# Kernel optimization log

Measured on AMD Instinct MI355X. Metric: run time of the kernel, lower is better.

Reference implementation:

```python
import jax, jax.numpy as jnp
import numpy as np

D_MODEL = 1024


def setup_inputs() -> dict:
    key = jax.random.key(0)
    ks = jax.random.split(key, 7)
    B, S, D = 4, 2048, D_MODEL
    scale = 1.0 / np.sqrt(D)
    inp = {
        "query": jax.random.normal(ks[0], (B, S, D), dtype=jnp.float32),
        "key": jax.random.normal(ks[1], (B, S, D), dtype=jnp.float32),
        "value": jax.random.normal(ks[2], (B, S, D), dtype=jnp.float32),
        # NOTE: original torch code applies query_projection to q, k AND v,
        # so only one projection weight (Wq) participates, plus output proj.
        "Wq": (jax.random.normal(ks[3], (D, D), dtype=jnp.float32) * scale),
        "bq": jnp.zeros((D,), dtype=jnp.float32),
        "Wo": (jax.random.normal(ks[4], (D, D), dtype=jnp.float32) * scale),
        "bo": jnp.zeros((D,), dtype=jnp.float32),
    }
    return inp


def reference(query, key, value, Wq, bq, Wo, bo):
    # Faithful to source: same projection (Wq, bq) used for q, k, v.
    q = jnp.einsum("bsd,de->bse", query, Wq) + bq   # (B, S, D)
    k = jnp.einsum("btd,de->bte", key, Wq) + bq     # (B, T, D)
    v = jnp.einsum("btd,de->bte", value, Wq) + bq   # (B, T, D)
    # No 1/sqrt(d) scaling in the original.
    score = jnp.einsum("bse,bte->bst", q, k)        # (B, S, T)
    weights = jax.nn.softmax(score, axis=-1)
    # Dropout is identity in eval / for a deterministic reference.
    ctx = jnp.einsum("bst,bte->bse", weights, v)    # (B, S, D)
    out = jnp.einsum("bse,ef->bsf", ctx, Wo) + bo   # (B, S, D)
    return (out, weights)
```

## Files before the change

kernel.cpp:

```cpp
#include <hip/hip_runtime.h>

typedef unsigned short u16;
typedef unsigned int u32;
typedef signed char i8;
typedef __bf16 bf16x8 __attribute__((ext_vector_type(8)));
typedef float f32x4 __attribute__((ext_vector_type(4)));
typedef int i32x4 __attribute__((ext_vector_type(4)));
typedef i8 i8x4 __attribute__((ext_vector_type(4)));
typedef u16 u16x8 __attribute__((ext_vector_type(8)));

#define AS1(p) ((const __attribute__((address_space(1))) void*)(p))
#define AS3(p) ((__attribute__((address_space(3))) void*)(p))

__device__ __forceinline__ u16 f2bf(float x) {
  u32 u = __float_as_uint(x);
  u32 r = u + 0x7fffu + ((u >> 16) & 1u);
  return (u16)(r >> 16);
}
__device__ __forceinline__ float bf2f(u16 h) {
  return __uint_as_float(((u32)h) << 16);
}

#define S_IN (8.0f / 127.0f)
#define S_W (0.25f / 127.0f)
#define S_QK (8.0f / 127.0f)
#define INV_S_IN (127.0f / 8.0f)
#define INV_S_W (508.0f)
#define INV_S_QK (127.0f / 8.0f)

__device__ __forceinline__ int2 q8i(float x, float inv_s) {
  float t = fminf(fmaxf(x * inv_s, -126.99f), 126.99f);
  float hf = rintf(t);
  float lf = fminf(fmaxf(rintf((t - hf) * 256.0f), -127.0f), 127.0f);
  return make_int2((int)hf, (int)lf);
}

__global__ __launch_bounds__(256) void prep_all(
    const float* __restrict__ q, const float* __restrict__ k,
    const float* __restrict__ value, const float* __restrict__ Wq,
    const float* __restrict__ Wo, i8* __restrict__ qh, i8* __restrict__ ql,
    i8* __restrict__ kh, i8* __restrict__ kl, u16* __restrict__ valT,
    i8* __restrict__ wqt_h, i8* __restrict__ wqt_l, u16* __restrict__ wot,
    u16* __restrict__ wq_b) {
  __shared__ float tileA[32][33];
  __shared__ float tileB[32][33];
  const int bid = blockIdx.x;
  const int tid = threadIdx.x;
  const int D = 1024;

  if (bid < 8192) {
    const int bx = bid & 31;
    const int by = (bid >> 5) & 63;
    const int bz = bid >> 11;
    const int tx = tid & 31, ty = tid >> 5;
    const int c0 = bx * 32, r0 = by * 32;
    const size_t zi = (size_t)bz * 2048 * 1024;
#pragma unroll
    for (int i = ty; i < 32; i += 8)
      tileA[i][tx] = value[zi + (size_t)(r0 + i) * D + (c0 + tx)];
    __syncthreads();
#pragma unroll
    for (int i = ty; i < 32; i += 8)
      valT[zi + (size_t)(c0 + i) * 2048 + (r0 + tx)] = f2bf(tileA[tx][i]);
  } else if (bid < 10240) {
    const int b2 = bid - 8192;
    const int n4 = 2097152;
    const int stride = 2048 * 256;
    for (int i = b2 * 256 + tid; i < n4; i += stride) {
      float4 x = ((const float4*)q)[i];
      float xs[4] = {x.x, x.y, x.z, x.w};
      i8x4 h, l;
#pragma unroll
      for (int e = 0; e < 4; ++e) {
        int2 r = q8i(xs[e], INV_S_IN);
        h[e] = (i8)r.x;
        l[e] = (i8)r.y;
      }
      ((i8x4*)qh)[i] = h;
      ((i8x4*)ql)[i] = l;
      x = ((const float4*)k)[i];
      float ys[4] = {x.x, x.y, x.z, x.w};
#pragma unroll
      for (int e = 0; e < 4; ++e) {
        int2 r = q8i(ys[e], INV_S_IN);
        h[e] = (i8)r.x;
        l[e] = (i8)r.y;
      }
      ((i8x4*)kh)[i] = h;
      ((i8x4*)kl)[i] = l;
    }
  } else {
    const int r = bid - 10240;
    const int bx = r & 31, by = r >> 5;
    const int tx = tid & 31, ty = tid >> 5;
    const int c0 = bx * 32, r0 = by * 32;
#pragma unroll
    for (int i = ty; i < 32; i += 8) {
      float xq = Wq[(size_t)(r0 + i) * D + c0 + tx];
      tileA[i][tx] = xq;
      wq_b[(size_t)(r0 + i) * D + c0 + tx] = f2bf(xq);
      tileB[i][tx] = Wo[(size_t)(r0 + i) * D + c0 + tx];
    }
    __syncthreads();
#pragma unroll
    for (int i = ty; i < 32; i += 8) {
      float x = tileA[tx][i];
      int2 rr = q8i(x, INV_S_W);
      size_t o = (size_t)(c0 + i) * D + r0 + tx;
      wqt_h[o] = (i8)rr.x;
      wqt_l[o] = (i8)rr.y;
      wot[o] = f2bf(tileB[tx][i]);
    }
  }
}

__global__ __launch_bounds__(256) void bqo_kernel(const float* __restrict__ bq,
                                                  const u16* __restrict__ wot,
                                                  const float* __restrict__ bo,
                                                  float* __restrict__ bqo,
                                                  int D) {
  const int f = blockIdx.x * 4 + (threadIdx.x >> 6);
  const int lane = threadIdx.x & 63;
  const u16* wr_ = wot + (size_t)f * D;
  float s = 0.f;
  for (int e = lane; e < D; e += 64) s += bq[e] * bf2f(wr_[e]);
#pragma unroll
  for (int off = 32; off; off >>= 1) s += __shfl_xor(s, off);
  if (lane == 0) bqo[f] = s + bo[f];
}

template <int EPI>
__global__ __launch_bounds__(256, 2) void gemm_bt(
    const u16* __restrict__ Ah, const u16* __restrict__ Bh,
    const float* __restrict__ bias, float* __restrict__ Cf,
    u16* __restrict__ Ch, int M, int N, int K,
    long long sA, long long sB, long long sC) {
  __shared__ alignas(16) u16 As[128 * 32];
  __shared__ alignas(16) u16 Bs[128 * 32];

  const int t = threadIdx.x;
  const int lane = t & 63;
  const int w = t >> 6;
  const int wr = w >> 1, wc = w & 1;

  const long long zb = blockIdx.z;
  const u16* pA = Ah + zb * sA;
  const u16* pB = Bh + zb * sB;

  const int m0 = blockIdx.x * 128;
  const int n0 = blockIdx.y * 128;

  f32x4 acc[4][4] = {};

  const int row0 = t >> 2;
  const int colS = (t & 3) * 8;
  const int lds0 = (t & ~63) * 8;
  const int lds1 = (256 + (t & ~63)) * 8;

  const size_t aoff0 = (size_t)(m0 + row0) * K + colS;
  const size_t aoff1 = (size_t)(m0 + row0 + 64) * K + colS;
  const size_t boff0 = (size_t)(n0 + row0) * K + colS;
  const size_t boff1 = (size_t)(n0 + row0 + 64) * K + colS;

  for (int k0 = 0; k0 < K; k0 += 32) {
    __syncthreads();
    __builtin_amdgcn_global_load_lds(AS1(pA + aoff0 + k0), AS3(&As[lds0]), 16, 0, 0);
    __builtin_amdgcn_global_load_lds(AS1(pA + aoff1 + k0), AS3(&As[lds1]), 16, 0, 0);
    __builtin_amdgcn_global_load_lds(AS1(pB + boff0 + k0), AS3(&Bs[lds0]), 16, 0, 0);
    __builtin_amdgcn_global_load_lds(AS1(pB + boff1 + k0), AS3(&Bs[lds1]), 16, 0, 0);
    __syncthreads();

    const int fr = lane & 15;
    const int kc = (lane >> 4) * 8;
    bf16x8 a[4], b[4];
#pragma unroll
    for (int i = 0; i < 4; ++i)
      a[i] = *(const bf16x8*)&As[(wr * 64 + i * 16 + fr) * 32 + kc];
#pragma unroll
    for (int j = 0; j < 4; ++j)
      b[j] = *(const bf16x8*)&Bs[(wc * 64 + j * 16 + fr) * 32 + kc];
#pragma unroll
    for (int i = 0; i < 4; ++i)
#pragma unroll
      for (int j = 0; j < 4; ++j)
        acc[i][j] = __builtin_amdgcn_mfma_f32_16x16x32_bf16(a[i], b[j], acc[i][j], 0, 0, 0);
  }

  const int er = (lane >> 4) * 4;
  const int ec = lane & 15;
#pragma unroll
  for (int j = 0; j < 4; ++j) {
    const int gcol = n0 + wc * 64 + j * 16 + ec;
    const float bv = bias ? bias[gcol] : 0.0f;
#pragma unroll
    for (int i = 0; i < 4; ++i) {
      const int grow0 = m0 + wr * 64 + i * 16 + er;
#pragma unroll
      for (int r = 0; r < 4; ++r) {
        const float x = acc[i][j][r] + bv;
        const size_t off = (size_t)zb * sC + (size_t)(grow0 + r) * N + gcol;
        if constexpr (EPI == 0) Cf[off] = x;
        else Ch[off] = f2bf(x);
      }
    }
  }
}

#define PH_PRE()                                                               \
  __builtin_amdgcn_s_barrier();                                                \
  asm volatile("s_waitcnt lgkmcnt(0)" ::: "memory");                           \
  __builtin_amdgcn_s_setprio(1)

#define PH_POST()                                                              \
  __builtin_amdgcn_s_setprio(0);                                               \
  __builtin_amdgcn_s_barrier()

#define STG_I(DSTBASE, SH, SL, ROWBASE, KREAL)                                 \
  do {                                                                         \
    const i8* s0_ = (sc < 4 ? (SH) : (SL)) +                                   \
                    (size_t)((ROWBASE) + sr) * K + (KREAL) + ((sc & 3) << 4);  \
    const i8* s1_ = s0_ + (size_t)64 * K;                                      \
    __builtin_amdgcn_global_load_lds(AS1(s0_), AS3(&lds8[(DSTBASE) + ldsB]), 16, 0, 0); \
    __builtin_amdgcn_global_load_lds(AS1(s1_), AS3(&lds8[(DSTBASE) + 8192 + ldsB]), 16, 0, 0); \
  } while (0)

#define LDA_I(BUF, QM)                                                         \
  do {                                                                         \
    const int base_ = (BUF) * 49152;                                           \
    _Pragma("unroll") for (int i_ = 0; i_ < 4; ++i_) {                         \
      const int r_ = (QM) * 128 + wr * 64 + i_ * 16 + fr;                      \
      ah_[i_] = *(const i32x4*)&lds8[base_ + r_ * 128 + ((ksl ^ (r_ & 7)) << 4)]; \
      al_[i_] = *(const i32x4*)&lds8[base_ + r_ * 128 + (((4 + ksl) ^ (r_ & 7)) << 4)]; \
    }                                                                          \
  } while (0)

#define LDB_I2(BUF)                                                            \
  do {                                                                         \
    const int base_ = (BUF) * 49152 + 32768;                                   \
    _Pragma("unroll") for (int j_ = 0; j_ < 2; ++j_) {                         \
      const int r_ = wc * 32 + j_ * 16 + fr;                                   \
      bh[j_] = *(const i32x4*)&lds8[base_ + r_ * 128 + ((ksl ^ (r_ & 7)) << 4)]; \
      bl[j_] = *(const i32x4*)&lds8[base_ + r_ * 128 + (((4 + ksl) ^ (r_ & 7)) << 4)]; \
    }                                                                          \
  } while (0)

#define MMA_I2(QM)                                                             \
  do {                                                                         \
    _Pragma("unroll") for (int j_ = 0; j_ < 2; ++j_) {                         \
      _Pragma("unroll") for (int i_ = 0; i_ < 4; ++i_) {                       \
        accH[(QM) * 4 + i_][j_] = __builtin_amdgcn_mfma_i32_16x16x64_i8(       \
            ah_[i_], bh[j_], accH[(QM) * 4 + i_][j_], 0, 0, 0);                \
        accX[(QM) * 4 + i_][j_] = __builtin_amdgcn_mfma_i32_16x16x64_i8(       \
            ah_[i_], bl[j_], accX[(QM) * 4 + i_][j_], 0, 0, 0);                \
        accX[(QM) * 4 + i_][j_] = __builtin_amdgcn_mfma_i32_16x16x64_i8(       \
            al_[i_], bh[j_], accX[(QM) * 4 + i_][j_], 0, 0, 0);                \
      }                                                                        \
    }                                                                          \
  } while (0)

template <int EPI>
__global__ __launch_bounds__(512, 2) void gemm8i(
    const i8* __restrict__ Ah, const i8* __restrict__ Al,
    const i8* __restrict__ Bh, const i8* __restrict__ Bl,
    const float* __restrict__ bias, float sAB, float* __restrict__ Cf,
    i8* __restrict__ Ch, i8* __restrict__ Cl, int M, int N, int K,
    long long sA, long long sB, long long sC) {
  extern __shared__ i8 lds8[];

  const int tt = threadIdx.x;
  const int lane = tt & 63;
  const int wv = tt >> 6;
  const int wr = wv >> 2;
  const int wc = wv & 3;
  const int fr = lane & 15;
  const int ksl = lane >> 4;

  const long long zb = blockIdx.z;
  const i8* pAh = Ah + zb * sA;
  const i8* pAl = Al + zb * sA;
  const i8* pBh = Bh + zb * sB;
  const i8* pBl = Bl + zb * sB;
  const int m0 = blockIdx.x * 256;
  const int n0 = blockIdx.y * 128;

  const int sr = tt >> 3;
  const int ss = tt & 7;
  const int sc = ss ^ (sr & 7);
  const int ldsB = (tt & ~63) * 16;

  i32x4 accH[8][2] = {};
  i32x4 accX[8][2] = {};
  i32x4 ah_[4], al_[4], bh[2], bl[2];

  const int NT = K / 64;
  const int NITER = NT / 2;

  STG_I(0, pAh, pAl, m0, 0);
  STG_I(16384, pAh, pAl, m0 + 128, 0);
  STG_I(32768, pBh, pBl, n0, 0);
  STG_I(49152, pAh, pAl, m0, 64);
  asm volatile("s_waitcnt vmcnt(2)" ::: "memory");
  __builtin_amdgcn_s_barrier();
  __builtin_amdgcn_sched_barrier(0);

  for (int it = 0; it < NITER; ++it) {
    const int t0 = 2 * it;
    const int k1 = (t0 + 1) * 64;
    const int k2 = (t0 + 2 < NT ? t0 + 2 : NT - 1) * 64;
    const int k3 = (t0 + 3 < NT ? t0 + 3 : NT - 1) * 64;

    LDA_I(0, 0);
    LDB_I2(0);
    STG_I(49152 + 16384, pAh, pAl, m0 + 128, k1);
    STG_I(49152 + 32768, pBh, pBl, n0, k1);
    PH_PRE();
    MMA_I2(0);
    PH_POST();

    LDA_I(0, 1);
    STG_I(0, pAh, pAl, m0, k2);
    PH_PRE();
    MMA_I2(1);
    __builtin_amdgcn_s_setprio(0);
    asm volatile("s_waitcnt vmcnt(2)" ::: "memory");
    __builtin_amdgcn_s_barrier();
    __builtin_amdgcn_sched_barrier(0);

    LDA_I(1, 0);
    LDB_I2(1);
    STG_I(16384, pAh, pAl, m0 + 128, k2);
    STG_I(32768, pBh, pBl, n0, k2);
    PH_PRE();
    MMA_I2(0);
    PH_POST();

    LDA_I(1, 1);
    STG_I(49152, pAh, pAl, m0, k3);
    PH_PRE();
    MMA_I2(1);
    __builtin_amdgcn_s_setprio(0);
    asm volatile("s_waitcnt vmcnt(2)" ::: "memory");
    __builtin_amdgcn_s_barrier();
    __builtin_amdgcn_sched_barrier(0);
  }

  const int er = (lane >> 4) * 4;
  const int ec = lane & 15;
#pragma unroll
  for (int fi = 0; fi < 8; ++fi) {
    const int grow0 = m0 + (fi >> 2) * 128 + wr * 64 + (fi & 3) * 16 + er;
#pragma unroll
    for (int j = 0; j < 2; ++j) {
      const int gcol = n0 + wc * 32 + j * 16 + ec;
      const float bv = bias ? bias[gcol] : 0.0f;
#pragma unroll
      for (int r = 0; r < 4; ++r) {
        const float x =
            sAB * ((float)accH[fi][j][r] + (float)accX[fi][j][r] * 0.00390625f) + bv;
        const size_t off = (size_t)zb * sC + (size_t)(grow0 + r) * N + gcol;
        if constexpr (EPI == 0) {
          Cf[off] = x;
        } else {
          int2 qq = q8i(x, INV_S_QK);
          Ch[off] = (i8)qq.x;
          Cl[off] = (i8)qq.y;
        }
      }
    }
  }
}

#define STG_P(DSTBASE, SRC, ROWBASE, KREAL)                                    \
  do {                                                                         \
    const u16* s0_ = (SRC) + (size_t)((ROWBASE) + sr) * K + (KREAL) + (sc << 3); \
    const u16* s1_ = s0_ + (size_t)64 * K;                                     \
    __builtin_amdgcn_global_load_lds(AS1(s0_), AS3(&lds[(DSTBASE) + ldsW]), 16, 0, 0); \
    __builtin_amdgcn_global_load_lds(AS1(s1_), AS3(&lds[(DSTBASE) + 4096 + ldsW]), 16, 0, 0); \
  } while (0)

#define LDA_P(BUF, QM, S, DST)                                                 \
  do {                                                                         \
    const int base_ = (BUF) * 24576 + (QM) * 8192;                             \
    _Pragma("unroll") for (int i_ = 0; i_ < 4; ++i_) {                         \
      const int r_ = wr * 64 + i_ * 16 + fr;                                   \
      DST[i_] = *(const bf16x8*)&lds[base_ + r_ * 64 + (((((S) * 4 + ksl)) ^ (r_ & 7)) << 3)]; \
    }                                                                          \
  } while (0)

#define LDB_P(BUF, S, DST)                                                     \
  do {                                                                         \
    const int base_ = (BUF) * 24576 + 16384;                                   \
    _Pragma("unroll") for (int j_ = 0; j_ < 2; ++j_) {                         \
      const int r_ = wc * 32 + j_ * 16 + fr;                                   \
      DST[j_] = *(const bf16x8*)&lds[base_ + r_ * 64 + (((((S) * 4 + ksl)) ^ (r_ & 7)) << 3)]; \
    }                                                                          \
  } while (0)

#define MMA_P(QM, A_, B_)                                                      \
  do {                                                                         \
    _Pragma("unroll") for (int i_ = 0; i_ < 4; ++i_) {                         \
      _Pragma("unroll") for (int j_ = 0; j_ < 2; ++j_) {                       \
        acc[(QM) * 4 + i_][j_] = __builtin_amdgcn_mfma_f32_16x16x32_bf16(      \
            A_[i_], B_[j_], acc[(QM) * 4 + i_][j_], 0, 0, 0);                  \
      }                                                                        \
    }                                                                          \
  } while (0)

template <int EPI>
__global__ __launch_bounds__(512, 2) void gemm8p(
    const u16* __restrict__ A, const u16* __restrict__ B,
    const float* __restrict__ bias, float* __restrict__ Cf,
    u16* __restrict__ Ch, int M, int N, int K,
    long long sA, long long sB, long long sC) {
  extern __shared__ u16 lds[];

  const int tt = threadIdx.x;
  const int lane = tt & 63;
  const int wv = tt >> 6;
  const int wr = wv >> 2;
  const int wc = wv & 3;
  const int fr = lane & 15;
  const int ksl = lane >> 4;

  const long long zb = blockIdx.z;
  const u16* pA = A + zb * sA;
  const u16* pB = B + zb * sB;
  const int m0 = blockIdx.x * 256;
  const int n0 = blockIdx.y * 128;

  const int sr = tt >> 3;
  const int ss = tt & 7;
  const int sc = ss ^ (sr & 7);
  const int ldsW = (tt & ~63) * 8;

  f32x4 acc[8][2] = {};
  bf16x8 a0[4], a1[4], b0[2], b1[2];

  const int NT = K / 64;

  STG_P(16384, pB, n0, 0);
  STG_P(0, pA, m0, 0);
  STG_P(8192, pA, m0 + 128, 0);
  asm volatile("s_waitcnt vmcnt(2)" ::: "memory");
  __builtin_amdgcn_s_barrier();
  __builtin_amdgcn_sched_barrier(0);

  for (int it = 0; it < NT; ++it) {
    const int cur = it & 1;
    const int nb = (cur ^ 1) * 24576;
    const int kn = (it + 1 < NT ? it + 1 : NT - 1) * 64;

    LDA_P(cur, 0, 0, a0);
    LDA_P(cur, 0, 1, a1);
    LDB_P(cur, 0, b0);
    LDB_P(cur, 1, b1);
    STG_P(nb + 16384, pB, n0, kn);
    STG_P(nb + 0, pA, m0, kn);
    PH_PRE();
    MMA_P(0, a0, b0);
    MMA_P(0, a1, b1);
    __builtin_amdgcn_s_setprio(0);
    asm volatile("s_waitcnt vmcnt(4)" ::: "memory");
    __builtin_amdgcn_s_barrier();
    __builtin_amdgcn_sched_barrier(0);

    LDA_P(cur, 1, 0, a0);
    LDA_P(cur, 1, 1, a1);
    STG_P(nb + 8192, pA, m0 + 128, kn);
    PH_PRE();
    MMA_P(1, a0, b0);
    MMA_P(1, a1, b1);
    __builtin_amdgcn_s_setprio(0);
    asm volatile("s_waitcnt vmcnt(2)" ::: "memory");
    __builtin_amdgcn_s_barrier();
    __builtin_amdgcn_sched_barrier(0);
  }

  const int er = (lane >> 4) * 4;
  const int ec = lane & 15;
#pragma unroll
  for (int fi = 0; fi < 8; ++fi) {
    const int qm = fi >> 2, i = fi & 3;
    const int grow0 = m0 + qm * 128 + wr * 64 + i * 16 + er;
#pragma unroll
    for (int j = 0; j < 2; ++j) {
      const int gcol = n0 + wc * 32 + j * 16 + ec;
      const float bv = bias ? bias[gcol] : 0.0f;
#pragma unroll
      for (int r = 0; r < 4; ++r) {
        const float x = acc[fi][j][r] + bv;
        const size_t off = (size_t)zb * sC + (size_t)(grow0 + r) * N + gcol;
        if constexpr (EPI == 0) Cf[off] = x;
        else Ch[off] = f2bf(x);
      }
    }
  }
}

__global__ __launch_bounds__(256) void softmax_rows_v(float* __restrict__ S,
                                                      u16* __restrict__ P) {
  const int T = 2048;
  const size_t row = blockIdx.x;
  float* sr = S + row * T;
  u16* prow = P + row * T;
  const int t = threadIdx.x;
  const int w = t >> 6, lane = t & 63;
  __shared__ float red[8];

  float4 r0 = ((const float4*)(sr + t * 8))[0];
  float4 r1 = ((const float4*)(sr + t * 8))[1];
  float v[8] = {r0.x, r0.y, r0.z, r0.w, r1.x, r1.y, r1.z, r1.w};
  float mx = -1e30f;
#pragma unroll
  for (int i = 0; i < 8; ++i) mx = fmaxf(mx, v[i]);
#pragma unroll
  for (int off = 32; off; off >>= 1) mx = fmaxf(mx, __shfl_xor(mx, off));
  if (lane == 0) red[w] = mx;
  __syncthreads();
  mx = fmaxf(fmaxf(red[0], red[1]), fmaxf(red[2], red[3]));

  float s = 0.f;
#pragma unroll
  for (int i = 0; i < 8; ++i) {
    v[i] = __expf(v[i] - mx);
    s += v[i];
  }
#pragma unroll
  for (int off = 32; off; off >>= 1) s += __shfl_xor(s, off);
  if (lane == 0) red[4 + w] = s;
  __syncthreads();
  s = (red[4] + red[5]) + (red[6] + red[7]);
  const float inv = 1.0f / s;

  u16x8 pv;
#pragma unroll
  for (int i = 0; i < 8; ++i) {
    v[i] *= inv;
    pv[i] = f2bf(v[i]);
  }
  float4* wr4 = (float4*)(sr + t * 8);
  wr4[0] = make_float4(v[0], v[1], v[2], v[3]);
  wr4[1] = make_float4(v[4], v[5], v[6], v[7]);
  ((u16x8*)prow)[t] = pv;
}

extern "C" void kernel_launch(void* const* d_in, const int* in_sizes, int n_in,
                              void* d_out, int out_size, void* d_ws,
                              size_t ws_size, hipStream_t stream) {
  (void)in_sizes; (void)n_in; (void)out_size; (void)ws_size;
  const float* query = (const float*)d_in[0];
  const float* key   = (const float*)d_in[1];
  const float* value = (const float*)d_in[2];
  const float* Wq    = (const float*)d_in[3];
  const float* bq    = (const float*)d_in[4];
  const float* Wo    = (const float*)d_in[5];
  const float* bo    = (const float*)d_in[6];

  const int S = 2048, D = 1024;
  const size_t n = (size_t)4 * S * D;

  float* out = (float*)d_out;
  float* wts = out + n;

  char* ws = (char*)d_ws;
  i8* wqt_h = (i8*)(ws);
  i8* wqt_l = (i8*)(ws + (1ull << 20));
  u16* wot  = (u16*)(ws + (2ull << 20));
  u16* wq_b = (u16*)(ws + (4ull << 20));
  u16* wqoT = (u16*)(ws + (6ull << 20));
  float* bqo = (float*)(ws + (8ull << 20));
  i8* QKh = (i8*)(ws + (9ull << 20));
  i8* QKl = (i8*)(ws + (25ull << 20));
  u16* tmp = (u16*)(ws + (41ull << 20));
  u16* P = (u16*)(ws + (9ull << 20));

  i8* ah = (i8*)wts;
  i8* al = ah + 2 * n;
  u16* valT = (u16*)out;

  hipFuncSetAttribute((const void*)&gemm8i<2>,
                      hipFuncAttributeMaxDynamicSharedMemorySize, 98304);
  hipFuncSetAttribute((const void*)&gemm8i<0>,
                      hipFuncAttributeMaxDynamicSharedMemorySize, 98304);
  hipFuncSetAttribute((const void*)&gemm8p<1>,
                      hipFuncAttributeMaxDynamicSharedMemorySize, 98304);
  hipFuncSetAttribute((const void*)&gemm8p<0>,
                      hipFuncAttributeMaxDynamicSharedMemorySize, 98304);

  prep_all<<<11264, 256, 0, stream>>>(query, key, value, Wq, Wo, ah, al,
                                      ah + n, al + n, valT, wqt_h, wqt_l, wot,
                                      wq_b);
  gemm_bt<1><<<dim3(8, 8, 1), 256, 0, stream>>>(
      wot, wq_b, nullptr, nullptr, wqoT, 1024, 1024, 1024, 0, 0, 0);
  bqo_kernel<<<256, 256, 0, stream>>>(bq, wot, bo, bqo, D);
  gemm8i<2><<<dim3(64, 8, 1), 512, 98304, stream>>>(
      ah, al, wqt_h, wqt_l, bq, S_IN * S_W, nullptr, QKh, QKl,
      16384, 1024, 1024, 0, 0, 0);
  gemm8i<0><<<dim3(8, 16, 4), 512, 98304, stream>>>(
      QKh, QKl, QKh + n, QKl + n, nullptr, S_QK * S_QK, wts, nullptr, nullptr,
      2048, 2048, 1024, (long long)S * D, (long long)S * D, (long long)S * S);
  softmax_rows_v<<<8192, 256, 0, stream>>>(wts, P);
  gemm8p<1><<<dim3(8, 8, 4), 512, 98304, stream>>>(
      P, valT, nullptr, nullptr, tmp, 2048, 1024, 2048, (long long)S * S,
      (long long)D * S, (long long)S * D);
  gemm8p<0><<<dim3(32, 8, 1), 512, 98304, stream>>>(
      tmp, wqoT, bqo, out, nullptr, 8192, 1024, 1024, 0, 0, 0);
}
```

Baseline: 274.5 us.

## Restructure int8 and bf16 GEMM main loops to prefetch two k-tiles ahead

Both GEMM kernels drop the ping-pong phase structure with setprio and per-phase barriers. Each iteration now loads all A/B fragments from LDS into separate register sets, runs all MFMAs, then issues the global->LDS loads for the tile two steps ahead, with vmcnt(6) waits. The aim is to keep two k-tiles in flight and cut barriers per tile. The cost is more registers for the extra fragment arrays and the loss of the priority-based wave interleaving.

New measurement: 275.0 us. No clear change (+0.2%).

```diff
diff --git a/kernel.cpp b/kernel.cpp
--- a/kernel.cpp
+++ b/kernel.cpp
@@ -206,15 +206,6 @@
   }
 }
 
-#define PH_PRE()                                                               \
-  __builtin_amdgcn_s_barrier();                                                \
-  asm volatile("s_waitcnt lgkmcnt(0)" ::: "memory");                           \
-  __builtin_amdgcn_s_setprio(1)
-
-#define PH_POST()                                                              \
-  __builtin_amdgcn_s_setprio(0);                                               \
-  __builtin_amdgcn_s_barrier()
-
 #define STG_I(DSTBASE, SH, SL, ROWBASE, KREAL)                                 \
   do {                                                                         \
     const i8* s0_ = (sc < 4 ? (SH) : (SL)) +                                   \
@@ -224,36 +215,36 @@
     __builtin_amdgcn_global_load_lds(AS1(s1_), AS3(&lds8[(DSTBASE) + 8192 + ldsB]), 16, 0, 0); \
   } while (0)
 
-#define LDA_I(BUF, QM)                                                         \
+#define LDA_IV(BUF, QM, AH, AL)                                                \
   do {                                                                         \
     const int base_ = (BUF) * 49152;                                           \
     _Pragma("unroll") for (int i_ = 0; i_ < 4; ++i_) {                         \
       const int r_ = (QM) * 128 + wr * 64 + i_ * 16 + fr;                      \
-      ah_[i_] = *(const i32x4*)&lds8[base_ + r_ * 128 + ((ksl ^ (r_ & 7)) << 4)]; \
-      al_[i_] = *(const i32x4*)&lds8[base_ + r_ * 128 + (((4 + ksl) ^ (r_ & 7)) << 4)]; \
+      AH[i_] = *(const i32x4*)&lds8[base_ + r_ * 128 + ((ksl ^ (r_ & 7)) << 4)]; \
+      AL[i_] = *(const i32x4*)&lds8[base_ + r_ * 128 + (((4 + ksl) ^ (r_ & 7)) << 4)]; \
     }                                                                          \
   } while (0)
 
-#define LDB_I2(BUF)                                                            \
+#define LDB_IV(BUF)                                                            \
   do {                                                                         \
     const int base_ = (BUF) * 49152 + 32768;                                   \
     _Pragma("unroll") for (int j_ = 0; j_ < 2; ++j_) {                         \
-      const int r_ = wc * 32 + j_ * 16 + fr;                                   \
+      const int r_ = wc * 32 + (j_) * 16 + fr;                                 \
       bh[j_] = *(const i32x4*)&lds8[base_ + r_ * 128 + ((ksl ^ (r_ & 7)) << 4)]; \
       bl[j_] = *(const i32x4*)&lds8[base_ + r_ * 128 + (((4 + ksl) ^ (r_ & 7)) << 4)]; \
     }                                                                          \
   } while (0)
 
-#define MMA_I2(QM)                                                             \
+#define MMA_IV(QM, AH, AL)                                                     \
   do {                                                                         \
     _Pragma("unroll") for (int j_ = 0; j_ < 2; ++j_) {                         \
       _Pragma("unroll") for (int i_ = 0; i_ < 4; ++i_) {                       \
         accH[(QM) * 4 + i_][j_] = __builtin_amdgcn_mfma_i32_16x16x64_i8(       \
-            ah_[i_], bh[j_], accH[(QM) * 4 + i_][j_], 0, 0, 0);                \
+            AH[i_], bh[j_], accH[(QM) * 4 + i_][j_], 0, 0, 0);                 \
         accX[(QM) * 4 + i_][j_] = __builtin_amdgcn_mfma_i32_16x16x64_i8(       \
-            ah_[i_], bl[j_], accX[(QM) * 4 + i_][j_], 0, 0, 0);                \
+            AH[i_], bl[j_], accX[(QM) * 4 + i_][j_], 0, 0, 0);                 \
         accX[(QM) * 4 + i_][j_] = __builtin_amdgcn_mfma_i32_16x16x64_i8(       \
-            al_[i_], bh[j_], accX[(QM) * 4 + i_][j_], 0, 0, 0);                \
+            AL[i_], bh[j_], accX[(QM) * 4 + i_][j_], 0, 0, 0);                 \
       }                                                                        \
     }                                                                          \
   } while (0)
@@ -290,7 +281,7 @@
 
   i32x4 accH[8][2] = {};
   i32x4 accX[8][2] = {};
-  i32x4 ah_[4], al_[4], bh[2], bl[2];
+  i32x4 ah0[4], al0[4], ah1[4], al1[4], bh[2], bl[2];
 
   const int NT = K / 64;
   const int NITER = NT / 2;
@@ -299,49 +290,41 @@
   STG_I(16384, pAh, pAl, m0 + 128, 0);
   STG_I(32768, pBh, pBl, n0, 0);
   STG_I(49152, pAh, pAl, m0, 64);
-  asm volatile("s_waitcnt vmcnt(2)" ::: "memory");
+  STG_I(49152 + 16384, pAh, pAl, m0 + 128, 64);
+  STG_I(49152 + 32768, pBh, pBl, n0, 64);
+  asm volatile("s_waitcnt vmcnt(6)" ::: "memory");
   __builtin_amdgcn_s_barrier();
-  __builtin_amdgcn_sched_barrier(0);
 
   for (int it = 0; it < NITER; ++it) {
     const int t0 = 2 * it;
-    const int k1 = (t0 + 1) * 64;
     const int k2 = (t0 + 2 < NT ? t0 + 2 : NT - 1) * 64;
     const int k3 = (t0 + 3 < NT ? t0 + 3 : NT - 1) * 64;
 
-    LDA_I(0, 0);
-    LDB_I2(0);
-    STG_I(49152 + 16384, pAh, pAl, m0 + 128, k1);
-    STG_I(49152 + 32768, pBh, pBl, n0, k1);
-    PH_PRE();
-    MMA_I2(0);
-    PH_POST();
-
-    LDA_I(0, 1);
+    LDA_IV(0, 0, ah0, al0);
+    LDB_IV(0);
+    LDA_IV(0, 1, ah1, al1);
+    MMA_IV(0, ah0, al0);
+    MMA_IV(1, ah1, al1);
+    asm volatile("s_waitcnt lgkmcnt(0)" ::: "memory");
+    __builtin_amdgcn_s_barrier();
     STG_I(0, pAh, pAl, m0, k2);
-    PH_PRE();
-    MMA_I2(1);
-    __builtin_amdgcn_s_setprio(0);
-    asm volatile("s_waitcnt vmcnt(2)" ::: "memory");
-    __builtin_amdgcn_s_barrier();
-    __builtin_amdgcn_sched_barrier(0);
-
-    LDA_I(1, 0);
-    LDB_I2(1);
     STG_I(16384, pAh, pAl, m0 + 128, k2);
     STG_I(32768, pBh, pBl, n0, k2);
-    PH_PRE();
-    MMA_I2(0);
-    PH_POST();
-
-    LDA_I(1, 1);
+    asm volatile("s_waitcnt vmcnt(6)" ::: "memory");
+    __builtin_amdgcn_s_barrier();
+
+    LDA_IV(1, 0, ah0, al0);
+    LDB_IV(1);
+    LDA_IV(1, 1, ah1, al1);
+    MMA_IV(0, ah0, al0);
+    MMA_IV(1, ah1, al1);
+    asm volatile("s_waitcnt lgkmcnt(0)" ::: "memory");
+    __builtin_amdgcn_s_barrier();
     STG_I(49152, pAh, pAl, m0, k3);
-    PH_PRE();
-    MMA_I2(1);
-    __builtin_amdgcn_s_setprio(0);
-    asm volatile("s_waitcnt vmcnt(2)" ::: "memory");
+    STG_I(49152 + 16384, pAh, pAl, m0 + 128, k3);
+    STG_I(49152 + 32768, pBh, pBl, n0, k3);
+    asm volatile("s_waitcnt vmcnt(6)" ::: "memory");
     __builtin_amdgcn_s_barrier();
-    __builtin_amdgcn_sched_barrier(0);
   }
 
   const int er = (lane >> 4) * 4;
@@ -434,46 +417,41 @@
   const int ldsW = (tt & ~63) * 8;
 
   f32x4 acc[8][2] = {};
-  bf16x8 a0[4], a1[4], b0[2], b1[2];
+  bf16x8 a0[4], a1[4], a2[4], a3[4], b0[2], b1[2];
 
   const int NT = K / 64;
 
   STG_P(16384, pB, n0, 0);
   STG_P(0, pA, m0, 0);
   STG_P(8192, pA, m0 + 128, 0);
-  asm volatile("s_waitcnt vmcnt(2)" ::: "memory");
+  STG_P(24576 + 16384, pB, n0, 64);
+  STG_P(24576 + 0, pA, m0, 64);
+  STG_P(24576 + 8192, pA, m0 + 128, 64);
+  asm volatile("s_waitcnt vmcnt(6)" ::: "memory");
   __builtin_amdgcn_s_barrier();
-  __builtin_amdgcn_sched_barrier(0);
 
   for (int it = 0; it < NT; ++it) {
     const int cur = it & 1;
-    const int nb = (cur ^ 1) * 24576;
-    const int kn = (it + 1 < NT ? it + 1 : NT - 1) * 64;
+    const int nb = cur * 24576;
+    const int kf = (it + 2 < NT ? it + 2 : NT - 1) * 64;
 
     LDA_P(cur, 0, 0, a0);
     LDA_P(cur, 0, 1, a1);
     LDB_P(cur, 0, b0);
     LDB_P(cur, 1, b1);
-    STG_P(nb + 16384, pB, n0, kn);
-    STG_P(nb + 0, pA, m0, kn);
-    PH_PRE();
+    LDA_P(cur, 1, 0, a2);
+    LDA_P(cur, 1, 1, a3);
     MMA_P(0, a0, b0);
     MMA_P(0, a1, b1);
-    __builtin_amdgcn_s_setprio(0);
-    asm volatile("s_waitcnt vmcnt(4)" ::: "memory");
+    MMA_P(1, a2, b0);
+    MMA_P(1, a3, b1);
+    asm volatile("s_waitcnt lgkmcnt(0)" ::: "memory");
     __builtin_amdgcn_s_barrier();
-    __builtin_amdgcn_sched_barrier(0);
-
-    LDA_P(cur, 1, 0, a0);
-    LDA_P(cur, 1, 1, a1);
-    STG_P(nb + 8192, pA, m0 + 128, kn);
-    PH_PRE();
-    MMA_P(1, a0, b0);
-    MMA_P(1, a1, b1);
-    __builtin_amdgcn_s_setprio(0);
-    asm volatile("s_waitcnt vmcnt(2)" ::: "memory");
+    STG_P(nb + 16384, pB, n0, kf);
+    STG_P(nb + 0, pA, m0, kf);
+    STG_P(nb + 8192, pA, m0 + 128, kf);
+    asm volatile("s_waitcnt vmcnt(6)" ::: "memory");
     __builtin_amdgcn_s_barrier();
-    __builtin_amdgcn_sched_barrier(0);
   }
 
   const int er = (lane >> 4) * 4;
```
